# Optimization experiments

Hardware: AMD Instinct MI355X
Metric: run time of the kernel (lower is better)

Reference implementation:

```python
import jax, jax.numpy as jnp
import numpy as np

TOP_K = 48
NUM_RBF = 16
NUM_RBF_SC = 8
MAXREL = 32
EDGE_F = 128
EPS_D = 1e-6
LN_EPS = 1e-5


def gather_nodes(nodes, idx):
    # nodes: [B, L, C], idx: [B, L, K] -> [B, L, K, C]
    return jax.vmap(lambda n, i: n[i])(nodes, idx)


def rbf(D, count):
    # D: [..., ] -> [..., count]; mu in [2, 22], sigma = 20/count
    mu = jnp.linspace(2.0, 22.0, count)
    sigma = (22.0 - 2.0) / count
    return jnp.exp(-(((D[..., None] - mu) / sigma) ** 2))


def layer_norm(x, g, b):
    mu = jnp.mean(x, -1, keepdims=True)
    var = jnp.mean((x - mu) ** 2, -1, keepdims=True)
    return g * (x - mu) / jnp.sqrt(var + LN_EPS) + b


def setup_inputs() -> dict:
    key = jax.random.key(0)
    ks = jax.random.split(key, 8)
    B, Lr = 1, 1024
    X = jax.random.normal(ks[0], (B, Lr, 37, 3), dtype=jnp.float32)
    mask = jnp.ones((B, Lr), dtype=jnp.float32)
    atom_mask = jnp.ones((B, Lr, 37), dtype=jnp.float32)
    residue_idx = jnp.arange(B * Lr, dtype=jnp.int64 if jax.config.jax_enable_x64 else jnp.int32).reshape(B, Lr)
    dihedral_mask = jnp.ones((B, Lr), dtype=jnp.float32)
    chain_labels = jnp.zeros((B, Lr), dtype=jnp.int32)
    W_pos = jax.random.normal(ks[1], (16, 2 * MAXREL + 2), dtype=jnp.float32) * 0.1
    b_pos = jnp.zeros((16,), dtype=jnp.float32)
    W_e = jax.random.normal(ks[2], (EDGE_F, 16 + NUM_RBF * 25), dtype=jnp.float32) * 0.05
    g_e = jnp.ones((EDGE_F,), dtype=jnp.float32)
    be_e = jnp.zeros((EDGE_F,), dtype=jnp.float32)
    W_s = jax.random.normal(ks[3], (EDGE_F, NUM_RBF_SC * 32 * 5), dtype=jnp.float32) * 0.05
    g_s = jnp.ones((EDGE_F,), dtype=jnp.float32)
    b_s = jnp.zeros((EDGE_F,), dtype=jnp.float32)
    return {"X": X, "L": 1024, "mask": mask, "atom_mask": atom_mask,
            "residue_idx": residue_idx, "dihedral_mask": dihedral_mask,
            "chain_labels": chain_labels, "W_pos": W_pos, "b_pos": b_pos,
            "W_e": W_e, "g_e": g_e, "be_e": be_e, "W_s": W_s, "g_s": g_s, "b_s": b_s}


def reference(X, L, mask, atom_mask, residue_idx, dihedral_mask, chain_labels,
              W_pos, b_pos, W_e, g_e, be_e, W_s, g_s, b_s):
    # Virtual Cb from ideal geometry
    b_v = X[:, :, 1, :] - X[:, :, 0, :]
    c_v = X[:, :, 2, :] - X[:, :, 1, :]
    a_v = jnp.cross(b_v, c_v)
    Cb = -0.58273431 * a_v + 0.56802827 * b_v - 0.54067466 * c_v + X[:, :, 1, :]
    Ca = X[:, :, 1, :]
    N = X[:, :, 0, :]
    C = X[:, :, 2, :]
    O = X[:, :, 4, :]

    # _dist: masked pairwise Ca distances + top-k smallest
    mask2d = mask[:, None, :] * mask[:, :, None]  # [B, L, L]
    dX = Ca[:, :, None, :] - Ca[:, None, :, :]
    D = mask2d * jnp.sqrt(jnp.sum(dX ** 2, -1) + EPS_D)
    D_max = jnp.max(D, -1, keepdims=True)
    D_adj = D + (1.0 - mask2d) * D_max
    neg_vals, E_idx = jax.lax.top_k(-D_adj, TOP_K)
    D_neighbors = -neg_vals  # [B, L, K]

    coords = {'N': N, 'Ca': Ca, 'C': C, 'O': O, 'Cb': Cb}
    pairs = [('N','N'),('C','C'),('O','O'),('Cb','Cb'),('Ca','N'),('Ca','C'),('Ca','O'),
             ('Ca','Cb'),('N','C'),('N','O'),('N','Cb'),('Cb','C'),('Cb','O'),('O','C'),
             ('N','Ca'),('C','Ca'),('O','Ca'),('Cb','Ca'),('C','N'),('O','N'),('Cb','N'),
             ('C','Cb'),('O','Cb'),('C','O')]
    A_st = jnp.stack([coords[a] for a, _ in pairs])  # [24, B, L, 3]
    B_st = jnp.stack([coords[b] for _, b in pairs])
    B_nb = jax.vmap(gather_nodes, (0, None))(B_st, E_idx)  # [24, B, L, K, 3]
    Dp = jnp.sqrt(jnp.sum((A_st[:, :, :, None, :] - B_nb) ** 2, -1) + EPS_D)  # [24,B,L,K]
    RBF_pairs = rbf(Dp, NUM_RBF)  # [24, B, L, K, 16]
    Bt, Lr, K = E_idx.shape
    RBF_pairs = jnp.moveaxis(RBF_pairs, 0, 3).reshape(Bt, Lr, K, 24 * NUM_RBF)
    RBF_all = jnp.concatenate([rbf(D_neighbors, NUM_RBF), RBF_pairs], -1)  # [B,L,K,400]

    # Positional encodings
    ri_nb = gather_nodes(residue_idx[..., None], E_idx)[..., 0]  # [B,L,K]
    offset = residue_idx[:, :, None] - ri_nb
    ch_nb = gather_nodes(chain_labels[..., None], E_idx)[..., 0]
    E_chains = (chain_labels[:, :, None] - ch_nb == 0).astype(jnp.int32)
    d = jnp.clip(offset + MAXREL, 0, 2 * MAXREL) * E_chains + (1 - E_chains) * (2 * MAXREL + 1)
    d_onehot = jax.nn.one_hot(d, 2 * MAXREL + 2, dtype=jnp.float32)
    E_positional = d_onehot @ W_pos.T + b_pos
    E = jnp.concatenate([E_positional, RBF_all], -1)  # [B,L,K,416]

    # Sidechain RBFs on the first min(100, K) neighbors
    Ks = min(100, K)
    E_idx_sub = E_idx[:, :, :Ks]
    am_g = gather_nodes(atom_mask, E_idx_sub)  # [B,L,Ks,37]
    S = X[:, :, 5:37, :]  # [B,L,32,3]
    S_nb = gather_nodes(S.reshape(Bt, Lr, 32 * 3), E_idx_sub).reshape(Bt, Lr, Ks, 32, 3)
    anchors = jnp.stack([N, Ca, C, O, Cb], 2)  # [B,L,5,3], anchor order matches loop order
    Ds = jnp.sqrt(jnp.sum((anchors[:, :, None, :, None, :] - S_nb[:, :, :, None, :, :]) ** 2, -1) + EPS_D)
    # Ds: [B,L,Ks,5,32]; rbf_side -> [B,L,Ks,5,32,8]; masked by neighbor atom mask
    RBF_s = rbf(Ds, NUM_RBF_SC) * am_g[:, :, :, None, 5:37, None]
    E_s = RBF_s.reshape(Bt, Lr, Ks, 5 * 32 * NUM_RBF_SC)  # [B,L,Ks,1280]

    E_s = layer_norm(E_s @ W_s.T, g_s, b_s)
    E = layer_norm(E @ W_e.T, g_e, be_e)
    return (E, E_idx, E_s, E_idx_sub)
```

## Files before the change

kernel.cpp:

```cpp
#include <hip/hip_runtime.h>
#include <math.h>

#define LRES 1024
#define TOPK 48
#define NEDGE (LRES*TOPK)

typedef short short8 __attribute__((ext_vector_type(8)));
typedef float f32x4  __attribute__((ext_vector_type(4)));

#define OUT_E     0
#define OUT_EIDX  6291456
#define OUT_ES    6340608
#define OUT_EIDX2 12632064

#define WS_COORDS 0
#define WS_DNB    15360
#define WS_EIDX   64512
#define WS_WPE    113664
#define WS_WPS    140288

#define DE 1.06666667f
#define QE 0.10273976f
#define DS 1.14285714f
#define QS 0.07337053f

__constant__ int PA[24] = {0,2,3,4,1,1,1,1,0,0,0,4,4,3,0,2,3,4,2,3,4,2,3,2};
__constant__ int PB[24] = {0,2,3,4,0,2,3,4,2,3,4,2,3,2,1,1,1,1,0,0,0,4,4,3};

__device__ inline short f2bf(float f) {
    unsigned u = __float_as_uint(f);
    unsigned r = (u + 0x7FFFu + ((u >> 16) & 1u)) >> 16;
    return (short)r;
}

__device__ inline short8 pack8(const float* fv) {
    union { short8 s; unsigned u[4]; } r;
    #pragma unroll
    for (int i = 0; i < 4; ++i)
        r.u[i] = __builtin_amdgcn_perm(__float_as_uint(fv[2*i+1]),
                                       __float_as_uint(fv[2*i]), 0x07060302u);
    return r.s;
}

__device__ __forceinline__ void ln_write(const f32x4* acc, float* op,
                                         const float* gv, const float* bv,
                                         int l16, int quad) {
    #pragma unroll
    for (int r = 0; r < 4; ++r) {
        float s = 0.f, s2 = 0.f;
        #pragma unroll
        for (int nt = 0; nt < 8; ++nt) { float x = acc[nt][r]; s += x; s2 = fmaf(x, x, s2); }
        #pragma unroll
        for (int m = 1; m <= 8; m <<= 1) {
            s  += __shfl_xor(s,  m);
            s2 += __shfl_xor(s2, m);
        }
        float mu = s * 0.0078125f;
        float rs = rsqrtf(fmaf(s2, 0.0078125f, -mu*mu) + 1e-5f);
        float* row = op + (quad*4 + r)*128 + l16;
        #pragma unroll
        for (int nt = 0; nt < 8; ++nt)
            row[nt*16] = gv[nt]*(acc[nt][r] - mu)*rs + bv[nt];
    }
}

__global__ __launch_bounds__(256) void k_pre(const float* __restrict__ X,
                                             const float* __restrict__ mask,
                                             const float* __restrict__ We,
                                             const float* __restrict__ Ws,
                                             float* __restrict__ coords,
                                             short* __restrict__ WpE,
                                             short* __restrict__ WpS,
                                             float* __restrict__ Dnb,
                                             int* __restrict__ Eidx,
                                             float* __restrict__ out) {
    int blk = blockIdx.x, t = threadIdx.x;
    if (blk < 256) {
        __shared__ float sCa[LRES*3];
        __shared__ float sM[LRES];
        for (int j = t; j < LRES; j += 256) {
            sCa[j*3+0] = X[j*111 + 3];
            sCa[j*3+1] = X[j*111 + 4];
            sCa[j*3+2] = X[j*111 + 5];
            sM[j] = mask[j];
        }
        __syncthreads();
        int w = t >> 6, lane = t & 63;
        int i = blk * 4 + w;
        float cx = sCa[i*3], cy = sCa[i*3+1], cz = sCa[i*3+2];
        float mi = sM[i];
        float dv[16], m2v[16];
        float lmax = -1e30f;
        #pragma unroll
        for (int s = 0; s < 16; ++s) {
            int j = s*64 + lane;
            float dx = cx - sCa[j*3], dy = cy - sCa[j*3+1], dz = cz - sCa[j*3+2];
            float d  = __builtin_amdgcn_sqrtf(dx*dx + dy*dy + dz*dz + 1e-6f);
            float m2 = mi * sM[j];
            dv[s] = m2 * d; m2v[s] = m2;
            lmax = fmaxf(lmax, dv[s]);
        }
        #pragma unroll
        for (int off = 32; off; off >>= 1) lmax = fmaxf(lmax, __shfl_xor(lmax, off));
        unsigned long long key[16];
        unsigned long long mkey = ~0ull; int mslot = 0;
        #pragma unroll
        for (int s = 0; s < 16; ++s) {
            float dadj = dv[s] + (1.0f - m2v[s]) * lmax;
            key[s] = (((unsigned long long)__float_as_uint(dadj)) << 10) | (unsigned)(s*64 + lane);
            if (key[s] < mkey) { mkey = key[s]; mslot = s; }
        }
        for (int it = 0; it < TOPK; ++it) {
            unsigned long long wk = mkey;
            #pragma unroll
            for (int off = 32; off; off >>= 1) {
                unsigned long long o = __shfl_xor(wk, off);
                wk = (o < wk) ? o : wk;
            }
            if (lane == 0) {
                int j = (int)(wk & 1023u);
                int id = i*TOPK + it;
                Dnb[id]  = __uint_as_float((unsigned)(wk >> 10));
                Eidx[id] = j;
                out[OUT_EIDX  + id] = (float)j;
                out[OUT_EIDX2 + id] = (float)j;
            }
            if (mkey == wk) {
                key[mslot] = ~0ull;
                mkey = ~0ull;
                #pragma unroll
                for (int s = 0; s < 16; ++s)
                    if (key[s] < mkey) { mkey = key[s]; mslot = s; }
            }
        }
    } else if (blk < 896) {
        int g = (blk - 256) * 256 + t;
        if (g < 104*512) {
            int j = g & 7, lane = (g >> 3) & 63, gg = g >> 9;
            int nt = gg & 7, ks = gg >> 3;
            int n = nt*16 + (lane & 15), k = ks*32 + (lane >> 4)*8 + j;
            WpE[g] = f2bf(We[n*416 + k]);
        }
        if (g < 320*512) {
            int j = g & 7, lane = (g >> 3) & 63, gg = g >> 9;
            int nt = gg & 7, ks = gg >> 3;
            int n = nt*16 + (lane & 15), k = ks*32 + (lane >> 4)*8 + j;
            WpS[g] = f2bf(Ws[n*1280 + k]);
        }
    } else {
        int r = (blk - 896) * 256 + t;
        if (r >= LRES) return;
        const float* xr = X + r * 111;
        float N[3], Ca[3], C[3], O[3], bv[3], cv[3], av[3];
        #pragma unroll
        for (int d = 0; d < 3; ++d) {
            N[d]  = xr[0*3 + d];  Ca[d] = xr[1*3 + d];
            C[d]  = xr[2*3 + d];  O[d]  = xr[4*3 + d];
            bv[d] = Ca[d] - N[d]; cv[d] = C[d] - Ca[d];
        }
        av[0] = bv[1]*cv[2] - bv[2]*cv[1];
        av[1] = bv[2]*cv[0] - bv[0]*cv[2];
        av[2] = bv[0]*cv[1] - bv[1]*cv[0];
        float* o = coords + r * 15;
        #pragma unroll
        for (int d = 0; d < 3; ++d) {
            float Cb = -0.58273431f*av[d] + 0.56802827f*bv[d] - 0.54067466f*cv[d] + Ca[d];
            o[0*3+d] = N[d]; o[1*3+d] = Ca[d]; o[2*3+d] = C[d];
            o[3*3+d] = O[d]; o[4*3+d] = Cb;
        }
    }
}

__global__ __launch_bounds__(256, 4) void k_edge(const float* __restrict__ coords,
                                                 const float* __restrict__ X,
                                                 const float* __restrict__ amask,
                                                 const short* __restrict__ WpE,
                                                 const short* __restrict__ WpS,
                                                 const float* __restrict__ Dnb,
                                                 const int* __restrict__ Eidx,
                                                 const int* __restrict__ ri,
                                                 const int* __restrict__ ch,
                                                 const float* __restrict__ Wpos,
                                                 const float* __restrict__ bpos,
                                                 const float* __restrict__ ge,
                                                 const float* __restrict__ be,
                                                 const float* __restrict__ gs,
                                                 const float* __restrict__ bs,
                                                 float* __restrict__ out) {
    __shared__ float smem[3872];
    int t = threadIdx.x;
    int w = t >> 6, lane = t & 63, quad = lane >> 4, l16 = lane & 15;
    int idB = (blockIdx.x >> 1) * 64;
    int i0  = idB / TOPK;

    if (!(blockIdx.x & 1)) {
        float* sA = smem;
        if (t < 30) {
            int rr = i0 + t/15; if (rr > LRES-1) rr = LRES-1;
            sA[t] = coords[rr*15 + t%15];
        }
        int id0 = idB + w*16;
        int id  = id0 + l16;
        int j   = Eidx[id];
        int ro  = (id/TOPK - i0)*15;
        const float* xp = X + (j*37 + 5)*3;
        const float* ap = amask + j*37 + 5;
        float S[8][3], am[8];
        #pragma unroll
        for (int q = 0; q < 8; ++q) {
            int s = q*4 + quad;
            S[q][0] = xp[s*3+0];
            S[q][1] = xp[s*3+1];
            S[q][2] = xp[s*3+2];
            am[q]   = ap[s];
        }
        __syncthreads();

        f32x4 acc[8] = {};
        const short8* bw = (const short8*)WpS + lane;
        for (int a = 0; a < 5; ++a) {
            if (a) __syncthreads();
            float A0 = sA[ro + a*3 + 0];
            float A1 = sA[ro + a*3 + 1];
            float A2 = sA[ro + a*3 + 2];
            #pragma unroll
            for (int q = 0; q < 8; ++q) {
                int ks = a*8 + q;
                float dx = A0 - S[q][0];
                float dy = A1 - S[q][1];
                float dz = A2 - S[q][2];
                float d  = __builtin_amdgcn_sqrtf(fmaf(dz,dz,fmaf(dy,dy,fmaf(dx,dx,1e-6f))));
                float u  = fmaf(d, 0.4f, -0.8f);
                float e0 = __expf(-u*u) * am[q];
                float g  = __expf(fmaf(2.0f*DS, u, -DS*DS));
                float fv[8];
                fv[0] = e0;
                #pragma unroll
                for (int r = 1; r < 8; ++r) { e0 *= g; g *= QS; fv[r] = e0; }
                short8 af = pack8(fv);
                #pragma unroll
                for (int nt = 0; nt < 8; ++nt) {
                    short8 b = bw[ks*512 + nt*64];
                    acc[nt] = __builtin_amdgcn_mfma_f32_16x16x32_bf16(af, b, acc[nt], 0,0,0);
                }
            }
        }
        float gv[8], bv[8];
        #pragma unroll
        for (int nt = 0; nt < 8; ++nt) { gv[nt] = gs[nt*16+l16]; bv[nt] = bs[nt*16+l16]; }
        ln_write(acc, out + OUT_ES + (size_t)id0*128, gv, bv, l16, quad);
    } else {
        float* sA    = smem;
        float* sB    = smem + 32;
        float* sdist = smem + 992;
        float* sposf = smem + 2720;
        int*   sdpos = (int*)(smem + 3808);

        if (t < 30) {
            int rr = i0 + t/15; if (rr > LRES-1) rr = LRES-1;
            sA[t] = coords[rr*15 + t%15];
        }
        if (t < 64) {
            int id = idB + t, i = id/TOPK, j = Eidx[id];
            int off = ri[i] - ri[j];
            sdpos[t] = (ch[i] == ch[j]) ? min(max(off + 32, 0), 64) : 65;
            sdist[t*27] = Dnb[id];
        }
        for (int it = t; it < 64*15; it += 256) {
            int e = it/15, q = it%15;
            int j = Eidx[idB + e];
            sB[e*15+q] = coords[j*15+q];
        }
        __syncthreads();
        for (int it = t; it < 64*24; it += 256) {
            int e = it/24, p = it%24, pa = PA[p], pb = PB[p];
            int roe = ((idB+e)/TOPK - i0)*15;
            float dx = sA[roe+pa*3+0] - sB[e*15+pb*3+0];
            float dy = sA[roe+pa*3+1] - sB[e*15+pb*3+1];
            float dz = sA[roe+pa*3+2] - sB[e*15+pb*3+2];
            sdist[e*27 + 1 + p] = __builtin_amdgcn_sqrtf(dx*dx + dy*dy + dz*dz + 1e-6f);
        }
        for (int it = t; it < 64*16; it += 256) {
            int e = it >> 4, c = it & 15;
            sposf[e*17 + c] = Wpos[c*66 + sdpos[e]] + bpos[c];
        }
        __syncthreads();

        f32x4 acc[8] = {};
        const short8* bw = (const short8*)WpE + lane;
        float rb = (quad & 1) ? 8.0f*DE : 0.0f;
        int e = w*16 + l16;
        for (int ks = 0; ks < 13; ++ks) {
            float fv[8];
            if (ks == 0 && quad < 2) {
                #pragma unroll
                for (int j = 0; j < 8; ++j) fv[j] = sposf[e*17 + quad*8 + j];
            } else {
                int p = (ks == 0) ? 0 : (2*ks - 1 + (quad >> 1));
                float d = sdist[e*27 + p];
                float u = fmaf(d, 0.8f, -1.6f) - rb;
                float e0 = __expf(-u*u);
                float g  = __expf(fmaf(2.0f*DE, u, -DE*DE));
                fv[0] = e0;
                #pragma unroll
                for (int r = 1; r < 8; ++r) { e0 *= g; g *= QE; fv[r] = e0; }
            }
            short8 af = pack8(fv);
            #pragma unroll
            for (int nt = 0; nt < 8; ++nt) {
                short8 b = bw[ks*512 + nt*64];
                acc[nt] = __builtin_amdgcn_mfma_f32_16x16x32_bf16(af, b, acc[nt], 0,0,0);
            }
        }
        int id0 = idB + w*16;
        float gv[8], bv[8];
        #pragma unroll
        for (int nt = 0; nt < 8; ++nt) { gv[nt] = ge[nt*16+l16]; bv[nt] = be[nt*16+l16]; }
        ln_write(acc, out + OUT_E + (size_t)id0*128, gv, bv, l16, quad);
    }
}

extern "C" void kernel_launch(void* const* d_in, const int* in_sizes, int n_in,
                              void* d_out, int out_size, void* d_ws, size_t ws_size,
                              hipStream_t stream) {
    (void)in_sizes; (void)n_in; (void)out_size; (void)ws_size;
    const float* X     = (const float*)d_in[0];
    const float* mask  = (const float*)d_in[2];
    const float* amask = (const float*)d_in[3];
    const int*   ri    = (const int*)d_in[4];
    const int*   ch    = (const int*)d_in[6];
    const float* Wpos  = (const float*)d_in[7];
    const float* bpos  = (const float*)d_in[8];
    const float* We    = (const float*)d_in[9];
    const float* ge    = (const float*)d_in[10];
    const float* be    = (const float*)d_in[11];
    const float* Ws    = (const float*)d_in[12];
    const float* gs    = (const float*)d_in[13];
    const float* bs    = (const float*)d_in[14];

    float* out    = (float*)d_out;
    float* ws     = (float*)d_ws;
    float* coords = ws + WS_COORDS;
    float* Dnb    = ws + WS_DNB;
    int*   Eidx   = (int*)(ws + WS_EIDX);
    short* WpE    = (short*)(ws + WS_WPE);
    short* WpS    = (short*)(ws + WS_WPS);

    k_pre <<<dim3(900),  dim3(256), 0, stream>>>(X, mask, We, Ws, coords,
                                                 WpE, WpS, Dnb, Eidx, out);
    k_edge<<<dim3(1536), dim3(256), 0, stream>>>(coords, X, amask, WpE, WpS,
                                                 Dnb, Eidx, ri, ch, Wpos, bpos,
                                                 ge, be, gs, bs, out);
}
```

Before: 221.3 us.

## Double-buffer packed weights in LDS via async global_load_lds

Weight fragments for both edge GEMMs are now staged into a double-buffered LDS tile with asynchronous global-to-LDS loads, overlapping the next k-slice fetch with current MFMA work instead of every wave reading weights straight from global memory. The sidechain weight packing is re-indexed so each lane reads a contiguous run of 8 sidechain atoms, which makes the coordinate loads contiguous. The backbone path drops the precomputed distance and positional tables in shared memory and computes them per lane inside the loop. This adds a block barrier for every k-slice, and there is a risk of LDS hazards because no explicit wait on the async loads is visible.

```diff
diff --git a/kernel.cpp b/kernel.cpp
--- a/kernel.cpp
+++ b/kernel.cpp
@@ -7,6 +7,7 @@
 
 typedef short short8 __attribute__((ext_vector_type(8)));
 typedef float f32x4  __attribute__((ext_vector_type(4)));
+typedef unsigned int u32;
 
 #define OUT_E     0
 #define OUT_EIDX  6291456
@@ -40,6 +41,12 @@
         r.u[i] = __builtin_amdgcn_perm(__float_as_uint(fv[2*i+1]),
                                        __float_as_uint(fv[2*i]), 0x07060302u);
     return r.s;
+}
+
+__device__ __forceinline__ void gload16(const void* g, void* l) {
+    __builtin_amdgcn_global_load_lds(
+        (const __attribute__((address_space(1))) u32*)g,
+        (__attribute__((address_space(3))) u32*)l, 16, 0, 0);
 }
 
 __device__ __forceinline__ void ln_write(const f32x4* acc, float* op,
@@ -144,7 +151,9 @@
         if (g < 320*512) {
             int j = g & 7, lane = (g >> 3) & 63, gg = g >> 9;
             int nt = gg & 7, ks = gg >> 3;
-            int n = nt*16 + (lane & 15), k = ks*32 + (lane >> 4)*8 + j;
+            int a = ks >> 3, q = ks & 7, quad = lane >> 4;
+            int n = nt*16 + (lane & 15);
+            int k = a*256 + quad*64 + q*8 + j;
             WpS[g] = f2bf(Ws[n*1280 + k]);
         }
     } else {
@@ -170,6 +179,13 @@
         }
     }
 }
+
+#define STAGE(Wsrc, buf, kss) do {                                              \
+    gload16((const short*)(Wsrc) + (((kss)*8 + w)*512)     + lane*8,            \
+            &sBuf[buf][w*512]);                                                 \
+    gload16((const short*)(Wsrc) + (((kss)*8 + w + 4)*512) + lane*8,            \
+            &sBuf[buf][(w+4)*512]);                                             \
+} while (0)
 
 __global__ __launch_bounds__(256, 4) void k_edge(const float* __restrict__ coords,
                                                  const float* __restrict__ X,
@@ -187,118 +203,119 @@
                                                  const float* __restrict__ gs,
                                                  const float* __restrict__ bs,
                                                  float* __restrict__ out) {
-    __shared__ float smem[3872];
+    __shared__ float smemF[992];
+    __shared__ __align__(16) short sBuf[2][4096];
     int t = threadIdx.x;
     int w = t >> 6, lane = t & 63, quad = lane >> 4, l16 = lane & 15;
     int idB = (blockIdx.x >> 1) * 64;
     int i0  = idB / TOPK;
 
     if (!(blockIdx.x & 1)) {
-        float* sA = smem;
+        float* sA = smemF;
         if (t < 30) {
             int rr = i0 + t/15; if (rr > LRES-1) rr = LRES-1;
             sA[t] = coords[rr*15 + t%15];
         }
         int id0 = idB + w*16;
         int id  = id0 + l16;
-        int j   = Eidx[id];
+        int jn  = Eidx[id];
         int ro  = (id/TOPK - i0)*15;
-        const float* xp = X + (j*37 + 5)*3;
-        const float* ap = amask + j*37 + 5;
-        float S[8][3], am[8];
-        #pragma unroll
-        for (int q = 0; q < 8; ++q) {
-            int s = q*4 + quad;
-            S[q][0] = xp[s*3+0];
-            S[q][1] = xp[s*3+1];
-            S[q][2] = xp[s*3+2];
-            am[q]   = ap[s];
-        }
+        const float* xp = X + jn*111 + 15 + quad*24;
+        const float* ap = amask + jn*37 + 5 + quad*8;
+        float Sf[24], am[8];
+        #pragma unroll
+        for (int c = 0; c < 24; ++c) Sf[c] = xp[c];
+        #pragma unroll
+        for (int c = 0; c < 8; ++c)  am[c] = ap[c];
+
+        STAGE(WpS, 0, 0);
         __syncthreads();
 
         f32x4 acc[8] = {};
-        const short8* bw = (const short8*)WpS + lane;
-        for (int a = 0; a < 5; ++a) {
-            if (a) __syncthreads();
-            float A0 = sA[ro + a*3 + 0];
-            float A1 = sA[ro + a*3 + 1];
-            float A2 = sA[ro + a*3 + 2];
+        int cur = 0;
+        #pragma unroll 1
+        for (int ks = 0; ks < 40; ++ks) {
+            if (ks < 39) STAGE(WpS, cur ^ 1, ks + 1);
+            int a = ks >> 3, q = ks & 7;
+            float dx = sA[ro + a*3 + 0] - Sf[q*3 + 0];
+            float dy = sA[ro + a*3 + 1] - Sf[q*3 + 1];
+            float dz = sA[ro + a*3 + 2] - Sf[q*3 + 2];
+            float d  = __builtin_amdgcn_sqrtf(fmaf(dz,dz,fmaf(dy,dy,fmaf(dx,dx,1e-6f))));
+            float u  = fmaf(d, 0.4f, -0.8f);
+            float e0 = __expf(-u*u) * am[q];
+            float g  = __expf(fmaf(2.0f*DS, u, -DS*DS));
+            float fv[8];
+            fv[0] = e0;
             #pragma unroll
-            for (int q = 0; q < 8; ++q) {
-                int ks = a*8 + q;
-                float dx = A0 - S[q][0];
-                float dy = A1 - S[q][1];
-                float dz = A2 - S[q][2];
-                float d  = __builtin_amdgcn_sqrtf(fmaf(dz,dz,fmaf(dy,dy,fmaf(dx,dx,1e-6f))));
-                float u  = fmaf(d, 0.4f, -0.8f);
-                float e0 = __expf(-u*u) * am[q];
-                float g  = __expf(fmaf(2.0f*DS, u, -DS*DS));
-                float fv[8];
-                fv[0] = e0;
-                #pragma unroll
-                for (int r = 1; r < 8; ++r) { e0 *= g; g *= QS; fv[r] = e0; }
-                short8 af = pack8(fv);
-                #pragma unroll
-                for (int nt = 0; nt < 8; ++nt) {
-                    short8 b = bw[ks*512 + nt*64];
-                    acc[nt] = __builtin_amdgcn_mfma_f32_16x16x32_bf16(af, b, acc[nt], 0,0,0);
-                }
-            }
+            for (int r = 1; r < 8; ++r) { e0 *= g; g *= QS; fv[r] = e0; }
+            short8 af = pack8(fv);
+            const short8* bb = (const short8*)sBuf[cur];
+            #pragma unroll
+            for (int nt = 0; nt < 8; ++nt) {
+                short8 b = bb[nt*64 + lane];
+                acc[nt] = __builtin_amdgcn_mfma_f32_16x16x32_bf16(af, b, acc[nt], 0,0,0);
+            }
+            if (ks < 39) { __syncthreads(); cur ^= 1; }
         }
         float gv[8], bv[8];
         #pragma unroll
         for (int nt = 0; nt < 8; ++nt) { gv[nt] = gs[nt*16+l16]; bv[nt] = bs[nt*16+l16]; }
         ln_write(acc, out + OUT_ES + (size_t)id0*128, gv, bv, l16, quad);
     } else {
-        float* sA    = smem;
-        float* sB    = smem + 32;
-        float* sdist = smem + 992;
-        float* sposf = smem + 2720;
-        int*   sdpos = (int*)(smem + 3808);
+        float* sA = smemF;
+        float* sB = smemF + 32;
 
         if (t < 30) {
             int rr = i0 + t/15; if (rr > LRES-1) rr = LRES-1;
             sA[t] = coords[rr*15 + t%15];
         }
-        if (t < 64) {
-            int id = idB + t, i = id/TOPK, j = Eidx[id];
-            int off = ri[i] - ri[j];
-            sdpos[t] = (ch[i] == ch[j]) ? min(max(off + 32, 0), 64) : 65;
-            sdist[t*27] = Dnb[id];
-        }
         for (int it = t; it < 64*15; it += 256) {
-            int e = it/15, q = it%15;
-            int j = Eidx[idB + e];
-            sB[e*15+q] = coords[j*15+q];
-        }
+            int e2 = it/15, q2 = it%15;
+            int j2 = Eidx[idB + e2];
+            sB[e2*15+q2] = coords[j2*15+q2];
+        }
+        int id0 = idB + w*16;
+        int e   = w*16 + l16;
+        int id  = id0 + l16;
+        int jn  = Eidx[id];
+        int ii  = id / TOPK;
+        float dnb = Dnb[id];
+        int offr = ri[ii] - ri[jn];
+        int dpos = (ch[ii] == ch[jn]) ? min(max(offr + 32, 0), 64) : 65;
+        float pf[8];
+        #pragma unroll
+        for (int c = 0; c < 8; ++c) {
+            int cc = (quad & 1)*8 + c;
+            pf[c] = Wpos[cc*66 + dpos] + bpos[cc];
+        }
+        int roe = (ii - i0)*15;
+        float rb = (quad & 1) ? 8.0f*DE : 0.0f;
+
+        STAGE(WpE, 0, 0);
         __syncthreads();
-        for (int it = t; it < 64*24; it += 256) {
-            int e = it/24, p = it%24, pa = PA[p], pb = PB[p];
-            int roe = ((idB+e)/TOPK - i0)*15;
-            float dx = sA[roe+pa*3+0] - sB[e*15+pb*3+0];
-            float dy = sA[roe+pa*3+1] - sB[e*15+pb*3+1];
-            float dz = sA[roe+pa*3+2] - sB[e*15+pb*3+2];
-            sdist[e*27 + 1 + p] = __builtin_amdgcn_sqrtf(dx*dx + dy*dy + dz*dz + 1e-6f);
-        }
-        for (int it = t; it < 64*16; it += 256) {
-            int e = it >> 4, c = it & 15;
-            sposf[e*17 + c] = Wpos[c*66 + sdpos[e]] + bpos[c];
-        }
-        __syncthreads();
 
         f32x4 acc[8] = {};
-        const short8* bw = (const short8*)WpE + lane;
-        float rb = (quad & 1) ? 8.0f*DE : 0.0f;
-        int e = w*16 + l16;
+        int cur = 0;
+        #pragma unroll 1
         for (int ks = 0; ks < 13; ++ks) {
+            if (ks < 12) STAGE(WpE, cur ^ 1, ks + 1);
             float fv[8];
             if (ks == 0 && quad < 2) {
                 #pragma unroll
-                for (int j = 0; j < 8; ++j) fv[j] = sposf[e*17 + quad*8 + j];
+                for (int c = 0; c < 8; ++c) fv[c] = pf[c];
             } else {
-                int p = (ks == 0) ? 0 : (2*ks - 1 + (quad >> 1));
-                float d = sdist[e*27 + p];
-                float u = fmaf(d, 0.8f, -1.6f) - rb;
+                float d;
+                if (ks == 0) {
+                    d = dnb;
+                } else {
+                    int p  = 2*ks - 1 + (quad >> 1);
+                    int pa = PA[p], pb = PB[p];
+                    float dx = sA[roe+pa*3+0] - sB[e*15+pb*3+0];
+                    float dy = sA[roe+pa*3+1] - sB[e*15+pb*3+1];
+                    float dz = sA[roe+pa*3+2] - sB[e*15+pb*3+2];
+                    d = __builtin_amdgcn_sqrtf(dx*dx + dy*dy + dz*dz + 1e-6f);
+                }
+                float u  = fmaf(d, 0.8f, -1.6f) - rb;
                 float e0 = __expf(-u*u);
                 float g  = __expf(fmaf(2.0f*DE, u, -DE*DE));
                 fv[0] = e0;
@@ -306,13 +323,14 @@
                 for (int r = 1; r < 8; ++r) { e0 *= g; g *= QE; fv[r] = e0; }
             }
             short8 af = pack8(fv);
+            const short8* bb = (const short8*)sBuf[cur];
             #pragma unroll
             for (int nt = 0; nt < 8; ++nt) {
-                short8 b = bw[ks*512 + nt*64];
+                short8 b = bb[nt*64 + lane];
                 acc[nt] = __builtin_amdgcn_mfma_f32_16x16x32_bf16(af, b, acc[nt], 0,0,0);
             }
-        }
-        int id0 = idB + w*16;
+            if (ks < 12) { __syncthreads(); cur ^= 1; }
+        }
         float gv[8], bv[8];
         #pragma unroll
         for (int nt = 0; nt < 8; ++nt) { gv[nt] = ge[nt*16+l16]; bv[nt] = be[nt*16+l16]; }
```

After: 193.0 us. 1.15x faster.
